# Performance work log

Hardware: AMD Instinct MI355X
Metric: run time of the kernel (lower is better)

## Reference

```python
import jax, jax.numpy as jnp
import numpy as np

B, S, D, H = 2, 2048, 2048, 16
HD = D // H  # 128


def apply_rotary(xq, xk, cos, sin):
    # xq, xk: [B, S, H, HD]; cos, sin: [S, HD//2]
    def rot(x):
        xr = x.astype(jnp.float32).reshape(*x.shape[:-1], -1, 2)  # [B,S,H,HD/2,2]
        xe, xo = xr[..., 0], xr[..., 1]
        c = cos[None, :, None, :]
        s = sin[None, :, None, :]
        out_e = xe * c - xo * s
        out_o = xe * s + xo * c
        out = jnp.stack([out_e, out_o], axis=-1).reshape(x.shape)
        return out.astype(x.dtype)
    return rot(xq), rot(xk)


def setup_inputs() -> dict:
    key = jax.random.key(0)
    ks = jax.random.split(key, 8)
    x = jax.random.normal(ks[0], (B, S, D), dtype=jnp.float32)
    scale = 1.0 / np.sqrt(D)
    wq = jax.random.normal(ks[1], (D, D), dtype=jnp.float32) * scale
    wk = jax.random.normal(ks[2], (D, D), dtype=jnp.float32) * scale
    wv = jax.random.normal(ks[3], (D, D), dtype=jnp.float32) * scale
    wo = jax.random.normal(ks[4], (D, D), dtype=jnp.float32) * scale
    # RoPE frequencies (standard LLaMA): theta = 10000
    inv_freq = 1.0 / (10000.0 ** (np.arange(0, HD, 2, dtype=np.float32) / HD))
    t = np.arange(S, dtype=np.float32)
    ang = np.outer(t, inv_freq)  # [S, HD/2]
    freqs_cos = jnp.asarray(np.cos(ang))
    freqs_sin = jnp.asarray(np.sin(ang))
    # causal additive mask [1,1,S,S]
    neg = jnp.full((S, S), -1e9, dtype=jnp.float32)
    mask = jnp.triu(neg, k=1)[None, None, :, :]
    return {"x": x, "start_pos": 0, "freqs_cos": freqs_cos, "freqs_sin": freqs_sin,
            "mask": mask, "wq": wq, "wk": wk, "wv": wv, "wo": wo}


def reference(x, start_pos, freqs_cos, freqs_sin, mask, wq, wk, wv, wo):
    bsz, seqlen, dim = x.shape
    xq = (x @ wq.T).reshape(bsz, seqlen, H, HD)
    xk = (x @ wk.T).reshape(bsz, seqlen, H, HD)
    xv = (x @ wv.T).reshape(bsz, seqlen, H, HD)
    xq, xk = apply_rotary(xq, xk, freqs_cos, freqs_sin)
    # [B,H,S,HD]
    q = xq.transpose(0, 2, 1, 3)
    k = xk.transpose(0, 2, 1, 3)
    v = xv.transpose(0, 2, 1, 3)
    scores = jnp.einsum('bhqd,bhkd->bhqk', q, k) / jnp.sqrt(jnp.float32(HD))
    scores = scores + mask
    probs = jax.nn.softmax(scores.astype(jnp.float32), axis=-1).astype(q.dtype)
    out = jnp.einsum('bhqk,bhkd->bhqd', probs, v)
    out = out.transpose(0, 2, 1, 3).reshape(bsz, seqlen, dim)
    return out @ wo.T
```

## Files before the change

### kernel.cpp

```cpp
#include <hip/hip_runtime.h>
#include <cstdint>

typedef unsigned short u16;
typedef __attribute__((ext_vector_type(8))) short bf16x8;
typedef __attribute__((ext_vector_type(4))) float f32x4;

#define S_LEN 2048
#define DM    2048
#define NH    16
#define HDIM  128

__device__ __forceinline__ u16 f2bf(float f) {
  union { float f; unsigned u; } v; v.f = f;
  unsigned r = v.u + 0x7fffu + ((v.u >> 16) & 1u);
  return (u16)(r >> 16);
}
__device__ __forceinline__ float bf2f(u16 h) {
  union { unsigned u; float f; } v; v.u = ((unsigned)h) << 16;
  return v.f;
}

typedef __attribute__((address_space(3))) void lds_void_t;
typedef const __attribute__((address_space(1))) void gbl_void_t;
__device__ __forceinline__ void gload_lds16(const void* g, void* l) {
  __builtin_amdgcn_global_load_lds((gbl_void_t*)g, (lds_void_t*)l, 16, 0, 0);
}

#define VMCNTN(nn) asm volatile("s_waitcnt vmcnt(%0)" :: "n"(nn) : "memory")

__global__ void cvt5_k(const float* s0, u16* d0, int n0,
                       const float* s1, u16* d1, int n1,
                       const float* s2, u16* d2, int n2,
                       const float* s3, u16* d3, int n3,
                       const float* s4, u16* d4, int n4) {
  const int stride = gridDim.x * blockDim.x;
  const int tid = blockIdx.x * blockDim.x + threadIdx.x;
#define CVT(S, D, N)                                        \
  for (int i = tid; i < ((N) >> 2); i += stride) {          \
    float4 v = ((const float4*)(S))[i];                     \
    ushort4 o;                                              \
    o.x = f2bf(v.x); o.y = f2bf(v.y);                       \
    o.z = f2bf(v.z); o.w = f2bf(v.w);                       \
    ((ushort4*)(D))[i] = o;                                 \
  }
  CVT(s0, d0, n0) CVT(s1, d1, n1) CVT(s2, d2, n2)
  CVT(s3, d3, n3) CVT(s4, d4, n4)
#undef CVT
}

template <int BM, int BN, int M, int N, int K, typename CT, int MODE>
__global__ __launch_bounds__(512, 2) void gemm8(const u16* __restrict__ A,
                                                const u16* __restrict__ Bm,
                                                CT* __restrict__ C,
                                                const float* __restrict__ fc,
                                                const float* __restrict__ fs,
                                                u16* __restrict__ qtp,
                                                u16* __restrict__ ktp) {
  constexpr int PWM = BM / 2, PWN = BN / 4;
  constexpr int MR = PWM / 16, NR = PWN / 16;
  constexpr int LA = BM / 128, LB = BN / 128;
  constexpr int VM6 = 2 * (LA + LB);
  constexpr int nbn = N / BN, nbm = M / BM;
  constexpr int nwg = nbm * nbn;
  constexpr int GM = 8;
  __shared__ u16 sA[4 * BM * 32];
  __shared__ u16 sB[4 * BN * 32];

  const int t = threadIdx.x;
  const int lane = t & 63, wid = t >> 6;
  const int r0 = lane & 15, kq = lane >> 4;
  const int wr = wid >> 2, wc = wid & 3;

  const int bid = blockIdx.x;
  const int wgl = (bid & 7) * (nwg >> 3) + (bid >> 3);
  const int gid = wgl / (GM * nbn);
  const int rem = wgl % (GM * nbn);
  const long tile_m = (long)(gid * GM + (rem & (GM - 1))) * BM;
  const long tile_n = (long)(rem >> 3) * BN;

  constexpr int NT = K >> 6;
  constexpr int NITER = NT >> 1;

  const int swzcol = ((t & 3) ^ ((t >> 3) & 3)) * 8;
  const u16* gA = A + (tile_m + (t >> 2)) * (long)K + swzcol;
  const u16* gB = Bm + (tile_n + (t >> 2)) * (long)K + swzcol;

  auto stageA = [&](int kt, int kh) {
    u16* base = &sA[((kt & 1) * 2 + kh) * (BM * 32)] + wid * 512;
#pragma unroll
    for (int r = 0; r < LA; ++r)
      gload_lds16(gA + (long)(r * 128) * K + kt * 64 + kh * 32, base + r * 4096);
  };
  auto stageB = [&](int kt, int kh) {
    u16* base = &sB[((kt & 1) * 2 + kh) * (BN * 32)] + wid * 512;
#pragma unroll
    for (int r = 0; r < LB; ++r)
      gload_lds16(gB + (long)(r * 128) * K + kt * 64 + kh * 32, base + r * 4096);
  };

  const int rdslot = (kq ^ ((r0 >> 1) & 3)) * 8;
  const int aoff = (wr * PWM + r0) * 32 + rdslot;
  const int boff = (wc * PWN + r0) * 32 + rdslot;

  f32x4 acc[MR][NR];
#pragma unroll
  for (int m = 0; m < MR; ++m)
#pragma unroll
    for (int n = 0; n < NR; ++n) acc[m][n] = (f32x4){0.f, 0.f, 0.f, 0.f};

  stageA(0, 0); stageB(0, 0); stageA(0, 1); stageB(0, 1);
  stageA(1, 0); stageB(1, 0);
  VMCNTN(VM6);
  __builtin_amdgcn_s_barrier();

#define PH4(KT, KH, SKT, SKH)                                               \
  {                                                                         \
    const u16* ra = &sA[(((KT) & 1) * 2 + (KH)) * (BM * 32)] + aoff;        \
    const u16* rb = &sB[(((KT) & 1) * 2 + (KH)) * (BN * 32)] + boff;        \
    _Pragma("unroll") for (int m = 0; m < MR; ++m)                          \
        a[m] = *(const bf16x8*)(ra + m * 512);                              \
    _Pragma("unroll") for (int n = 0; n < NR; ++n)                          \
        b[n] = *(const bf16x8*)(rb + n * 512);                              \
    stageA(SKT, SKH);                                                       \
    stageB(SKT, SKH);                                                       \
    VMCNTN(VM6);                                                            \
    __builtin_amdgcn_s_barrier();                                           \
    __builtin_amdgcn_s_setprio(1);                                          \
    _Pragma("unroll") for (int m = 0; m < MR; ++m)                          \
        _Pragma("unroll") for (int n = 0; n < NR; ++n)                      \
            acc[m][n] = __builtin_amdgcn_mfma_f32_16x16x32_bf16(            \
                a[m], b[n], acc[m][n], 0, 0, 0);                            \
    __builtin_amdgcn_s_setprio(0);                                          \
    __builtin_amdgcn_s_barrier();                                           \
  }

  for (int it = 0; it < NITER; ++it) {
    const int kt0 = 2 * it, kt1 = 2 * it + 1;
    bf16x8 a[MR], b[NR];
    PH4(kt0, 0, kt1, 1);
    PH4(kt0, 1, kt0 + 2, 0);
    PH4(kt1, 0, kt0 + 2, 1);
    PH4(kt1, 1, kt0 + 3, 0);
  }
#undef PH4

  if constexpr (MODE == 1) {
    const int z = (int)(tile_n >> 11);
    if (z == 2) {
#pragma unroll
      for (int m = 0; m < MR; ++m)
#pragma unroll
        for (int n = 0; n < NR; ++n)
#pragma unroll
          for (int r = 0; r < 4; ++r) {
            long grow = tile_m + wr * PWM + m * 16 + kq * 4 + r;
            long gcol = tile_n + wc * PWN + n * 16 + r0;
            C[grow * N + gcol] = (CT)f2bf(acc[m][n][r]);
          }
    } else {
      const float qsc = 0.12751743202f;
#pragma unroll
      for (int m = 0; m < MR; ++m)
#pragma unroll
        for (int n = 0; n < NR; ++n)
#pragma unroll
          for (int r = 0; r < 4; ++r) {
            long grow = tile_m + wr * PWM + m * 16 + kq * 4 + r;
            long gcol = tile_n + wc * PWN + n * 16 + r0;
            int srow = (int)(grow & 2047), bidx = (int)(grow >> 11);
            int h = ((int)gcol >> 7) & 15, hd = (int)gcol & 127;
            float v = acc[m][n][r];
            float partner = __shfl_xor(v, 1);
            int hd2 = hd >> 1;
            float c = fc[srow * 64 + hd2], sn = fs[srow * 64 + hd2];
            float res = (r0 & 1) ? (partner * sn + v * c)
                                 : (v * c - partner * sn);
            if (z == 0) res *= qsc;
            u16* dst = z ? ktp : qtp;
            dst[((long)(bidx * 16 + h) * S_LEN + srow) * HDIM + hd] = f2bf(res);
          }
    }
  } else {
#pragma unroll
    for (int m = 0; m < MR; ++m)
#pragma unroll
      for (int n = 0; n < NR; ++n)
#pragma unroll
        for (int r = 0; r < 4; ++r) {
          long grow = tile_m + wr * PWM + m * 16 + kq * 4 + r;
          long gcol = tile_n + wc * PWN + n * 16 + r0;
          float v = acc[m][n][r];
          if constexpr (sizeof(CT) == 2) C[grow * N + gcol] = (CT)f2bf(v);
          else                           C[grow * N + gcol] = v;
        }
  }
}

__global__ void vtrans_k(const u16* __restrict__ qkv, u16* __restrict__ vt) {
  __shared__ u16 tile[64][65];
  int bh = blockIdx.z;
  int b = bh >> 4, h = bh & 15;
  int s0 = blockIdx.x * 64, d0 = blockIdx.y * 64;
  int tx = threadIdx.x, ty = threadIdx.y;
#pragma unroll
  for (int i = 0; i < 64; i += 4) {
    int s = s0 + ty + i;
    tile[ty + i][tx] = qkv[((long)(b * S_LEN + s)) * 6144 + 4096 + h * HDIM + d0 + tx];
  }
  __syncthreads();
#pragma unroll
  for (int i = 0; i < 64; i += 4) {
    int d = d0 + ty + i;
    vt[((long)bh * HDIM + d) * S_LEN + s0 + tx] = tile[tx][ty + i];
  }
}

__global__ __launch_bounds__(128) void flash_k(const u16* __restrict__ qt,
                                               const u16* __restrict__ kt,
                                               const u16* __restrict__ vt,
                                               u16* __restrict__ attn) {
  constexpr int PS = 40;
  __shared__ u16 pbuf[2][2][32 * PS];
  const int t = threadIdx.x, lane = t & 63, wid = t >> 6;
  const int r0 = lane & 15, kq = lane >> 4;
  const int bh = blockIdx.x, b = bh >> 4, h = bh & 15;
  const int tile = (gridDim.y - 1) - blockIdx.y;
  const int q0w = tile * 64 + wid * 32;
  const int crow = kq * 4;

  const u16* qb = qt + ((long)bh * S_LEN + q0w) * HDIM;
  const u16* kb = kt + (long)bh * S_LEN * HDIM;
  const u16* vb = vt + (long)bh * HDIM * S_LEN;
  u16* pb0 = &pbuf[0][wid][0];
  u16* pb1 = &pbuf[1][wid][0];

  bf16x8 aq[2][4];
#pragma unroll
  for (int qc = 0; qc < 2; ++qc)
#pragma unroll
    for (int kk = 0; kk < 4; ++kk)
      aq[qc][kk] = *(const bf16x8*)(qb + (qc * 16 + r0) * HDIM + kk * 32 + kq * 8);

  f32x4 o[2][8];
  float mrow[2] = {-1e30f, -1e30f}, lrow[2] = {0.f, 0.f};
#pragma unroll
  for (int qc = 0; qc < 2; ++qc)
#pragma unroll
    for (int dt = 0; dt < 8; ++dt) o[qc][dt] = (f32x4){0.f, 0.f, 0.f, 0.f};

  bf16x8 bkA[2][4], bkB[2][4], bvA[8], bvB[8];
  f32x4 saccA[2][2], saccB[2][2];

  auto loadK = [&](bf16x8 (&dst)[2][4], int kv) {
#pragma unroll
    for (int kc = 0; kc < 2; ++kc)
#pragma unroll
      for (int kk = 0; kk < 4; ++kk)
        dst[kc][kk] = *(const bf16x8*)(kb + (long)(kv + kc * 16 + r0) * HDIM + kk * 32 + kq * 8);
  };
  auto loadV = [&](bf16x8 (&dst)[8], int kv) {
#pragma unroll
    for (int dt = 0; dt < 8; ++dt)
      dst[dt] = *(const bf16x8*)(vb + (long)(dt * 16 + r0) * S_LEN + kv + kq * 8);
  };
  auto qk = [&](bf16x8 (&kf)[2][4], f32x4 (&sacc)[2][2]) {
    __builtin_amdgcn_s_setprio(1);
#pragma unroll
    for (int kc = 0; kc < 2; ++kc) {
      f32x4 a0 = (f32x4){0.f, 0.f, 0.f, 0.f};
      f32x4 a1 = (f32x4){0.f, 0.f, 0.f, 0.f};
#pragma unroll
      for (int kk = 0; kk < 4; ++kk) {
        a0 = __builtin_amdgcn_mfma_f32_16x16x32_bf16(kf[kc][kk], aq[0][kk], a0, 0, 0, 0);
        a1 = __builtin_amdgcn_mfma_f32_16x16x32_bf16(kf[kc][kk], aq[1][kk], a1, 0, 0, 0);
      }
      sacc[kc][0] = a0; sacc[kc][1] = a1;
    }
    __builtin_amdgcn_s_setprio(0);
  };
  auto softmax_store = [&](f32x4 (&sacc)[2][2], int kv0, u16* pb) {
    const bool diag = (kv0 == q0w);
#pragma unroll
    for (int qc = 0; qc < 2; ++qc) {
      float s[2][4];
#pragma unroll
      for (int kc = 0; kc < 2; ++kc)
#pragma unroll
        for (int r = 0; r < 4; ++r) {
          float v = sacc[kc][qc][r];
          if (diag && (kc * 16 + crow + r > qc * 16 + r0)) v = -1e30f;
          s[kc][r] = v;
        }
      float pm = fmaxf(fmaxf(fmaxf(s[0][0], s[0][1]), fmaxf(s[0][2], s[0][3])),
                       fmaxf(fmaxf(s[1][0], s[1][1]), fmaxf(s[1][2], s[1][3])));
      pm = fmaxf(pm, __shfl_xor(pm, 16));
      pm = fmaxf(pm, __shfl_xor(pm, 32));
      if (!__all(pm - mrow[qc] <= 11.5416f)) {
        float mnew = fmaxf(mrow[qc], pm);
        float co = exp2f(mrow[qc] - mnew);
        mrow[qc] = mnew;
        lrow[qc] *= co;
        float cod[4];
#pragma unroll
        for (int r = 0; r < 4; ++r)
          cod[r] = __shfl(co, (lane & 48) | (crow + r));
#pragma unroll
        for (int dt = 0; dt < 8; ++dt)
#pragma unroll
          for (int r = 0; r < 4; ++r)
            o[qc][dt][r] *= cod[r];
      }
      float p[2][4];
      float rs = 0.f;
#pragma unroll
      for (int kc = 0; kc < 2; ++kc)
#pragma unroll
        for (int r = 0; r < 4; ++r) {
          p[kc][r] = exp2f(s[kc][r] - mrow[qc]);
          rs += p[kc][r];
        }
      rs += __shfl_xor(rs, 16);
      rs += __shfl_xor(rs, 32);
      lrow[qc] += rs;
#pragma unroll
      for (int kc = 0; kc < 2; ++kc) {
        unsigned w0, w1;
        asm("v_cvt_pk_bf16_f32 %0, %1, %2" : "=v"(w0) : "v"(p[kc][0]), "v"(p[kc][1]));
        asm("v_cvt_pk_bf16_f32 %0, %1, %2" : "=v"(w1) : "v"(p[kc][2]), "v"(p[kc][3]));
        uint2 w; w.x = w0; w.y = w1;
        *(uint2*)(pb + (qc * 16 + r0) * PS + kc * 16 + crow) = w;
      }
    }
  };
  auto pv = [&](const u16* pb, bf16x8 (&bv)[8]) {
    bf16x8 pa0 = *(const bf16x8*)(pb + r0 * PS + kq * 8);
    bf16x8 pa1 = *(const bf16x8*)(pb + (16 + r0) * PS + kq * 8);
    __builtin_amdgcn_s_setprio(1);
#pragma unroll
    for (int dt = 0; dt < 8; ++dt) {
      o[0][dt] = __builtin_amdgcn_mfma_f32_16x16x32_bf16(pa0, bv[dt], o[0][dt], 0, 0, 0);
      o[1][dt] = __builtin_amdgcn_mfma_f32_16x16x32_bf16(pa1, bv[dt], o[1][dt], 0, 0, 0);
    }
    __builtin_amdgcn_s_setprio(0);
  };

  loadK(bkA, 0);
  if (32 <= q0w) loadK(bkB, 32);
  qk(bkA, saccA);
  int kv0 = 0;
  for (;;) {
    {
      const bool more = (kv0 + 32 <= q0w);
      loadV(bvA, kv0);
      softmax_store(saccA, kv0, pb0);
      if (more) qk(bkB, saccB);
      if (kv0 + 64 <= q0w) loadK(bkA, kv0 + 64);
      pv(pb0, bvA);
      kv0 += 32;
      if (!more) break;
    }
    {
      const bool more = (kv0 + 32 <= q0w);
      loadV(bvB, kv0);
      softmax_store(saccB, kv0, pb1);
      if (more) qk(bkA, saccA);
      if (kv0 + 64 <= q0w) loadK(bkB, kv0 + 64);
      pv(pb1, bvB);
      kv0 += 32;
      if (!more) break;
    }
  }

#pragma unroll
  for (int qc = 0; qc < 2; ++qc) {
    float linv[4];
#pragma unroll
    for (int r = 0; r < 4; ++r)
      linv[r] = 1.0f / __shfl(lrow[qc], (lane & 48) | (crow + r));
#pragma unroll
    for (int dt = 0; dt < 8; ++dt)
#pragma unroll
      for (int r = 0; r < 4; ++r) {
        int srow = q0w + qc * 16 + crow + r;
        attn[((long)(b * S_LEN + srow)) * DM + h * HDIM + dt * 16 + r0] =
            f2bf(o[qc][dt][r] * linv[r]);
      }
  }
}

extern "C" void kernel_launch(void* const* d_in, const int* in_sizes, int n_in,
                              void* d_out, int out_size, void* d_ws, size_t ws_size,
                              hipStream_t stream) {
  (void)in_sizes; (void)n_in; (void)out_size; (void)ws_size;
  const float* x  = (const float*)d_in[0];
  const float* fc = (const float*)d_in[2];
  const float* fs = (const float*)d_in[3];
  const float* wq = (const float*)d_in[5];
  const float* wk = (const float*)d_in[6];
  const float* wv = (const float*)d_in[7];
  const float* wo = (const float*)d_in[8];
  float* out = (float*)d_out;

  u16* xb   = (u16*)d_ws;
  u16* wqkv = xb + 8388608;
  u16* wob  = wqkv + 12582912;
  u16* qkv  = wob + 4194304;
  u16* qt   = qkv + 25165824;
  u16* kt   = qt + 8388608;
  u16* vt   = kt + 8388608;
  u16* attn = qkv;

  cvt5_k<<<2048, 256, 0, stream>>>(x, xb, 8388608,
                                   wq, wqkv, 4194304,
                                   wk, wqkv + 4194304, 4194304,
                                   wv, wqkv + 8388608, 4194304,
                                   wo, wob, 4194304);

  gemm8<128, 256, 4096, 6144, 2048, u16, 1><<<768, 512, 0, stream>>>(
      xb, wqkv, qkv, fc, fs, qt, kt);

  vtrans_k<<<dim3(32, 2, 32), dim3(64, 4), 0, stream>>>(qkv, vt);

  flash_k<<<dim3(32, 32), 128, 0, stream>>>(qt, kt, vt, attn);

  gemm8<128, 256, 4096, 2048, 2048, float, 0><<<256, 512, 0, stream>>>(
      attn, wob, out, nullptr, nullptr, nullptr, nullptr);
}
```

Measured before the change: 316.6 us.

## Replace four-slot LDS ring with double-buffered per-half-tile GEMM pipeline

Restructures the bf16 GEMM main loop from a four-slot LDS ring, unrolled by four phases, into a simple double buffer indexed per 32-wide K slice. Each step reads its fragments into registers and waits on lgkmcnt. It then barriers, issues the global-to-LDS prefetch two slices ahead into the buffer just consumed, and runs the MFMAs before waiting for the next slice. This halves the GEMM's shared-memory footprint and simplifies the loop. In exchange, the prefetch queue is shallower, so less global-load latency is hidden behind MFMA work.

```diff
diff --git a/kernel.cpp b/kernel.cpp
--- a/kernel.cpp
+++ b/kernel.cpp
@@ -27,6 +27,7 @@
 }
 
 #define VMCNTN(nn) asm volatile("s_waitcnt vmcnt(%0)" :: "n"(nn) : "memory")
+#define LGKMCNT0() asm volatile("s_waitcnt lgkmcnt(0)" ::: "memory")
 
 __global__ void cvt5_k(const float* s0, u16* d0, int n0,
                        const float* s1, u16* d1, int n1,
@@ -59,12 +60,13 @@
   constexpr int PWM = BM / 2, PWN = BN / 4;
   constexpr int MR = PWM / 16, NR = PWN / 16;
   constexpr int LA = BM / 128, LB = BN / 128;
-  constexpr int VM6 = 2 * (LA + LB);
+  constexpr int VMK = LA + LB;
+  constexpr int LDSA = BM * 32, LDSB = BN * 32;
   constexpr int nbn = N / BN, nbm = M / BM;
   constexpr int nwg = nbm * nbn;
   constexpr int GM = 8;
-  __shared__ u16 sA[4 * BM * 32];
-  __shared__ u16 sB[4 * BN * 32];
+  __shared__ u16 sA[2 * LDSA];
+  __shared__ u16 sB[2 * LDSB];
 
   const int t = threadIdx.x;
   const int lane = t & 63, wid = t >> 6;
@@ -78,24 +80,22 @@
   const long tile_m = (long)(gid * GM + (rem & (GM - 1))) * BM;
   const long tile_n = (long)(rem >> 3) * BN;
 
-  constexpr int NT = K >> 6;
-  constexpr int NITER = NT >> 1;
+  constexpr int NPH = K / 32;
 
   const int swzcol = ((t & 3) ^ ((t >> 3) & 3)) * 8;
   const u16* gA = A + (tile_m + (t >> 2)) * (long)K + swzcol;
   const u16* gB = Bm + (tile_n + (t >> 2)) * (long)K + swzcol;
 
-  auto stageA = [&](int kt, int kh) {
-    u16* base = &sA[((kt & 1) * 2 + kh) * (BM * 32)] + wid * 512;
+  auto stage = [&](int h) {
+    u16* ba = &sA[(h & 1) * LDSA] + wid * 512;
+    u16* bb = &sB[(h & 1) * LDSB] + wid * 512;
+    const long coff = (long)h * 32;
 #pragma unroll
     for (int r = 0; r < LA; ++r)
-      gload_lds16(gA + (long)(r * 128) * K + kt * 64 + kh * 32, base + r * 4096);
-  };
-  auto stageB = [&](int kt, int kh) {
-    u16* base = &sB[((kt & 1) * 2 + kh) * (BN * 32)] + wid * 512;
+      gload_lds16(gA + (long)(r * 128) * K + coff, ba + r * 4096);
 #pragma unroll
     for (int r = 0; r < LB; ++r)
-      gload_lds16(gB + (long)(r * 128) * K + kt * 64 + kh * 32, base + r * 4096);
+      gload_lds16(gB + (long)(r * 128) * K + coff, bb + r * 4096);
   };
 
   const int rdslot = (kq ^ ((r0 >> 1) & 3)) * 8;
@@ -108,41 +108,32 @@
 #pragma unroll
     for (int n = 0; n < NR; ++n) acc[m][n] = (f32x4){0.f, 0.f, 0.f, 0.f};
 
-  stageA(0, 0); stageB(0, 0); stageA(0, 1); stageB(0, 1);
-  stageA(1, 0); stageB(1, 0);
-  VMCNTN(VM6);
+  stage(0); stage(1);
+  VMCNTN(VMK);
   __builtin_amdgcn_s_barrier();
 
-#define PH4(KT, KH, SKT, SKH)                                               \
-  {                                                                         \
-    const u16* ra = &sA[(((KT) & 1) * 2 + (KH)) * (BM * 32)] + aoff;        \
-    const u16* rb = &sB[(((KT) & 1) * 2 + (KH)) * (BN * 32)] + boff;        \
-    _Pragma("unroll") for (int m = 0; m < MR; ++m)                          \
-        a[m] = *(const bf16x8*)(ra + m * 512);                              \
-    _Pragma("unroll") for (int n = 0; n < NR; ++n)                          \
-        b[n] = *(const bf16x8*)(rb + n * 512);                              \
-    stageA(SKT, SKH);                                                       \
-    stageB(SKT, SKH);                                                       \
-    VMCNTN(VM6);                                                            \
-    __builtin_amdgcn_s_barrier();                                           \
-    __builtin_amdgcn_s_setprio(1);                                          \
-    _Pragma("unroll") for (int m = 0; m < MR; ++m)                          \
-        _Pragma("unroll") for (int n = 0; n < NR; ++n)                      \
-            acc[m][n] = __builtin_amdgcn_mfma_f32_16x16x32_bf16(            \
-                a[m], b[n], acc[m][n], 0, 0, 0);                            \
-    __builtin_amdgcn_s_setprio(0);                                          \
-    __builtin_amdgcn_s_barrier();                                           \
-  }
-
-  for (int it = 0; it < NITER; ++it) {
-    const int kt0 = 2 * it, kt1 = 2 * it + 1;
+  for (int h = 0; h < NPH; ++h) {
+    const u16* ra = &sA[(h & 1) * LDSA] + aoff;
+    const u16* rb = &sB[(h & 1) * LDSB] + boff;
     bf16x8 a[MR], b[NR];
-    PH4(kt0, 0, kt1, 1);
-    PH4(kt0, 1, kt0 + 2, 0);
-    PH4(kt1, 0, kt0 + 2, 1);
-    PH4(kt1, 1, kt0 + 3, 0);
-  }
-#undef PH4
+#pragma unroll
+    for (int m = 0; m < MR; ++m) a[m] = *(const bf16x8*)(ra + m * 512);
+#pragma unroll
+    for (int n = 0; n < NR; ++n) b[n] = *(const bf16x8*)(rb + n * 512);
+    LGKMCNT0();
+    __builtin_amdgcn_s_barrier();
+    stage(h + 2);
+    __builtin_amdgcn_s_setprio(1);
+#pragma unroll
+    for (int m = 0; m < MR; ++m)
+#pragma unroll
+      for (int n = 0; n < NR; ++n)
+        acc[m][n] = __builtin_amdgcn_mfma_f32_16x16x32_bf16(a[m], b[n],
+                                                            acc[m][n], 0, 0, 0);
+    __builtin_amdgcn_s_setprio(0);
+    VMCNTN(VMK);
+    __builtin_amdgcn_s_barrier();
+  }
 
   if constexpr (MODE == 1) {
     const int z = (int)(tile_n >> 11);
```

Measured after the change: 319.0 us. No clear change (+0.8%).
